# Optimization experiments

Measured on AMD Instinct MI355X. Metric: run time of the kernel, lower is better.

## Reference

```python
import jax, jax.numpy as jnp
import numpy as np

C_IN = 512
C = 64        # per-head dim
N_HEAD = 8
B, S = 2, 2048


def setup_inputs() -> dict:
    key = jax.random.key(0)
    ks = jax.random.split(key, 9)
    scale = 1.0 / np.sqrt(C_IN)
    return {
        "x": jax.random.normal(ks[0], (B, S, C_IN), dtype=jnp.float32),
        "bias": jax.random.normal(ks[1], (B, N_HEAD, S, S), dtype=jnp.float32),
        "Wq": jax.random.normal(ks[2], (N_HEAD * C, C_IN), dtype=jnp.float32) * scale,
        "Wk": jax.random.normal(ks[3], (N_HEAD * C, C_IN), dtype=jnp.float32) * scale,
        "Wv": jax.random.normal(ks[4], (N_HEAD * C, C_IN), dtype=jnp.float32) * scale,
        "Wo": jax.random.normal(ks[5], (C_IN, N_HEAD * C), dtype=jnp.float32) * scale,
        "bo": jax.random.normal(ks[6], (C_IN,), dtype=jnp.float32) * 0.01,
        "Wg": jax.random.normal(ks[7], (N_HEAD * C, C_IN), dtype=jnp.float32) * scale,
        "bg": jax.random.normal(ks[8], (N_HEAD * C,), dtype=jnp.float32) * 0.01,
    }


def reference(x, bias, Wq, Wk, Wv, Wo, bo, Wg, bg):
    # x: [B, S, C_IN]; attn_dim=1 -> q/k/v axis is already at -2 after movedim.
    # Project and split heads: [B, S, H*C] -> [B, H, S, C]
    def split_heads(t):
        Bq, Sq, _ = t.shape
        return t.reshape(Bq, Sq, N_HEAD, C).transpose(0, 2, 1, 3)

    q = split_heads(x @ Wq.T) / jnp.sqrt(jnp.asarray(C, x.dtype))
    k = split_heads(x @ Wk.T)
    v = split_heads(x @ Wv.T)

    a = jnp.einsum("bhqc,bhkc->bhqk", q, k) + bias   # [B, H, S, S]
    a = jax.nn.softmax(a, axis=-1)
    o = jnp.einsum("bhqk,bhkc->bhqc", a, v)          # [B, H, S, C]

    # merge heads back: [B, S, H*C]
    o = o.transpose(0, 2, 1, 3).reshape(x.shape[0], x.shape[1], N_HEAD * C)
    g = jax.nn.sigmoid(x @ Wg.T + bg)
    o = g * o
    return o @ Wo.T + bo                              # [B, S, C_IN]
```

## Files before the change

### kernel.cpp

```cpp
#include <hip/hip_runtime.h>
#include <math.h>

#define BB 2
#define HH 8
#define SS 2048
#define CC 64
#define CIN 512
#define DDIM 512
#define MM (BB*SS)
#define KSPLIT 2
#define KDOM (SS / KSPLIT)
#define NCHUNK (KDOM / 64)

#define SOFTMAX_SHIFT 16.0f

using short8  = __attribute__((ext_vector_type(8))) short;
using float4v = __attribute__((ext_vector_type(4))) float;

__device__ __forceinline__ unsigned short tob(float f) {
    unsigned u = __float_as_uint(f);
    unsigned r = (u + 0x7fffu + ((u >> 16) & 1u)) >> 16;
    return (unsigned short)r;
}
__device__ __forceinline__ float fromb(unsigned short u) {
    return __uint_as_float(((unsigned)u) << 16);
}

__global__ __launch_bounds__(256) void convert_all(
    const float* __restrict__ x,
    const float* __restrict__ wq, const float* __restrict__ wk,
    const float* __restrict__ wv, const float* __restrict__ wg,
    const float* __restrict__ wo,
    unsigned short* __restrict__ xb,
    unsigned short* __restrict__ wqb, unsigned short* __restrict__ wkb,
    unsigned short* __restrict__ wvb, unsigned short* __restrict__ wgb,
    unsigned short* __restrict__ wob)
{
    const int NX4 = MM * CIN / 4;
    int i = blockIdx.x * blockDim.x + threadIdx.x;
    const float* src; unsigned short* dst; float scale = 1.0f; int off;
    if (i < NX4) { src = x; dst = xb; off = i; }
    else {
        int j = i - NX4;
        int seg = j >> 16;
        off = j & 65535;
        if      (seg == 0) { src = wq; dst = wqb; scale = 0.125f; }
        else if (seg == 1) { src = wk; dst = wkb; }
        else if (seg == 2) { src = wv; dst = wvb; }
        else if (seg == 3) { src = wg; dst = wgb; }
        else               { src = wo; dst = wob; }
    }
    float4 v = ((const float4*)src)[off];
    ushort4 o;
    o.x = tob(v.x * scale); o.y = tob(v.y * scale);
    o.z = tob(v.z * scale); o.w = tob(v.w * scale);
    ((ushort4*)dst)[off] = o;
}

__global__ __launch_bounds__(256) void proj_gemm(
    const unsigned short* __restrict__ X,
    const unsigned short* __restrict__ Wq,
    const unsigned short* __restrict__ Wk,
    const unsigned short* __restrict__ Wv,
    const unsigned short* __restrict__ Wg,
    const float* __restrict__ bg,
    unsigned short* __restrict__ Qd,
    unsigned short* __restrict__ Kd,
    unsigned short* __restrict__ Vd,
    unsigned short* __restrict__ Gd)
{
    __shared__ __align__(16) unsigned short At[64][72];
    __shared__ __align__(16) unsigned short Bt[64][72];

    int mode = blockIdx.z;
    const unsigned short* W = (mode == 0) ? Wq : (mode == 1) ? Wk : (mode == 2) ? Wv : Wg;

    int m0 = blockIdx.y * 64;
    int n0 = blockIdx.x * 64;
    int tid = threadIdx.x;
    int w = tid >> 6, lane = tid & 63;
    int quad = lane >> 4, l16 = lane & 15;
    int wm = w & 1, wn = w >> 1;

    float4v acc[2][2];
    for (int a = 0; a < 2; ++a) for (int c = 0; c < 2; ++c) acc[a][c] = (float4v)0.0f;

    for (int kc = 0; kc < CIN; kc += 64) {
        for (int it = 0; it < 2; ++it) {
            int idx = it * 2048 + tid * 8;
            int row = idx >> 6, col = idx & 63;
            *(short8*)&At[row][col] = *(const short8*)&X[(size_t)(m0 + row) * CIN + kc + col];
            *(short8*)&Bt[row][col] = *(const short8*)&W[(size_t)(n0 + row) * CIN + kc + col];
        }
        __syncthreads();
        for (int ks = 0; ks < 2; ++ks) {
            short8 a0 = *(const short8*)&At[wm * 32 + l16][ks * 32 + quad * 8];
            short8 a1 = *(const short8*)&At[wm * 32 + 16 + l16][ks * 32 + quad * 8];
            short8 b0 = *(const short8*)&Bt[wn * 32 + l16][ks * 32 + quad * 8];
            short8 b1 = *(const short8*)&Bt[wn * 32 + 16 + l16][ks * 32 + quad * 8];
            acc[0][0] = __builtin_amdgcn_mfma_f32_16x16x32_bf16(a0, b0, acc[0][0], 0, 0, 0);
            acc[0][1] = __builtin_amdgcn_mfma_f32_16x16x32_bf16(a0, b1, acc[0][1], 0, 0, 0);
            acc[1][0] = __builtin_amdgcn_mfma_f32_16x16x32_bf16(a1, b0, acc[1][0], 0, 0, 0);
            acc[1][1] = __builtin_amdgcn_mfma_f32_16x16x32_bf16(a1, b1, acc[1][1], 0, 0, 0);
        }
        __syncthreads();
    }

    if (mode == 2) {
        for (int a = 0; a < 2; ++a) for (int c = 0; c < 2; ++c)
            for (int r = 0; r < 4; ++r) {
                int ml = wm * 32 + a * 16 + quad * 4 + r;
                int nl = wn * 32 + c * 16 + l16;
                At[nl][ml] = tob(acc[a][c][r]);
            }
        __syncthreads();
        int bi = m0 >> 11, h = n0 >> 6, s0 = m0 & 2047;
        int crow = tid >> 2, seg = tid & 3;
        unsigned short* dp = Vd + (((size_t)(bi * HH + h) * CC) + crow) * SS + s0 + seg * 16;
        *(short8*)dp       = *(const short8*)&At[crow][seg * 16];
        *(short8*)(dp + 8) = *(const short8*)&At[crow][seg * 16 + 8];
        return;
    }

    for (int a = 0; a < 2; ++a) for (int c = 0; c < 2; ++c)
        for (int r = 0; r < 4; ++r) {
            int gm = m0 + wm * 32 + a * 16 + quad * 4 + r;
            int gn = n0 + wn * 32 + c * 16 + l16;
            float v = acc[a][c][r];
            if (mode <= 1) {
                int bi = gm >> 11, s = gm & 2047, h = gn >> 6, cc = gn & 63;
                unsigned short* d = (mode == 0) ? Qd : Kd;
                d[(((size_t)(bi * HH + h) * SS) + s) * CC + cc] = tob(v);
            } else {
                float g = 1.0f / (1.0f + __expf(-(v + bg[gn])));
                Gd[(size_t)gm * DDIM + gn] = tob(g);
            }
        }
}

__global__ __launch_bounds__(256) void attn_kernel(
    const unsigned short* __restrict__ Q,
    const unsigned short* __restrict__ K,
    const unsigned short* __restrict__ V,
    const float* __restrict__ bias,
    float* __restrict__ part,
    float* __restrict__ Ls)
{
    __shared__ __align__(16) unsigned short Kt[64][72];
    __shared__ __align__(16) unsigned short Vt[64][72];
    __shared__ __align__(16) unsigned short Pt[4][16][72];

    int qb = blockIdx.x * 64;
    int bh = blockIdx.y;
    int split = blockIdx.z;
    int ksbase = split * KDOM;
    int b = bh >> 3, h = bh & 7;
    int tid = threadIdx.x;
    int w = tid >> 6, lane = tid & 63;
    int quad = lane >> 4, l16 = lane & 15;

    const unsigned short* Qbh = Q + (size_t)bh * SS * CC;
    const unsigned short* Kbh = K + (size_t)bh * SS * CC + (size_t)ksbase * CC;
    const unsigned short* Vbh = V + (size_t)bh * CC * SS + ksbase;
    const float* biasbh = bias + (size_t)bh * SS * SS + ksbase;

    int qrow = qb + w * 16 + l16;
    short8 aq0 = *(const short8*)&Qbh[(size_t)qrow * CC + quad * 8];
    short8 aq1 = *(const short8*)&Qbh[(size_t)qrow * CC + 32 + quad * 8];

    float lsum[4] = {0.f, 0.f, 0.f, 0.f};
    float4v accO[4];
    for (int jn = 0; jn < 4; ++jn) accO[jn] = (float4v)0.0f;

    int srow0 = (tid * 8) >> 6,        scol0 = (tid * 8) & 63;
    int srow1 = (2048 + tid * 8) >> 6, scol1 = (2048 + tid * 8) & 63;

    const float* brow[4];
    for (int r = 0; r < 4; ++r)
        brow[r] = biasbh + (size_t)(qb + w * 16 + quad * 4 + r) * SS + l16;

    short8 pk0[2], pv0[2], pk1[2], pv1[2];
    float  bb0[4][4], bb1[4][4];
    pk0[0] = *(const short8*)&Kbh[(size_t)srow0 * CC + scol0];
    pk0[1] = *(const short8*)&Kbh[(size_t)srow1 * CC + scol1];
    pv0[0] = *(const short8*)&Vbh[(size_t)srow0 * SS + scol0];
    pv0[1] = *(const short8*)&Vbh[(size_t)srow1 * SS + scol1];
    for (int j = 0; j < 4; ++j)
        for (int r = 0; r < 4; ++r)
            bb0[j][r] = brow[r][j * 16];

#pragma unroll
    for (int c = 0; c < NCHUNK; ++c) {
        int kb  = c * 64;
        int kbn = (c + 1 < NCHUNK ? c + 1 : c) * 64;
        const bool even = (c & 1) == 0;
        short8* pkc = even ? pk0 : pk1;
        short8* pvc = even ? pv0 : pv1;
        short8* pkn = even ? pk1 : pk0;
        short8* pvn = even ? pv1 : pv0;
        float (*bbc)[4] = even ? bb0 : bb1;
        float (*bbn)[4] = even ? bb1 : bb0;

        __syncthreads();
        *(short8*)&Kt[srow0][scol0] = pkc[0];
        *(short8*)&Kt[srow1][scol1] = pkc[1];
        *(short8*)&Vt[srow0][scol0] = pvc[0];
        *(short8*)&Vt[srow1][scol1] = pvc[1];

        pkn[0] = *(const short8*)&Kbh[(size_t)(kbn + srow0) * CC + scol0];
        pkn[1] = *(const short8*)&Kbh[(size_t)(kbn + srow1) * CC + scol1];
        pvn[0] = *(const short8*)&Vbh[(size_t)srow0 * SS + kbn + scol0];
        pvn[1] = *(const short8*)&Vbh[(size_t)srow1 * SS + kbn + scol1];
        for (int j = 0; j < 4; ++j)
            for (int r = 0; r < 4; ++r)
                bbn[j][r] = brow[r][kbn + j * 16];

        __syncthreads();

        float4v sa[4];
        for (int j = 0; j < 4; ++j) sa[j] = (float4v)0.0f;
        for (int j = 0; j < 4; ++j) {
            short8 bk0 = *(const short8*)&Kt[j * 16 + l16][quad * 8];
            short8 bk1 = *(const short8*)&Kt[j * 16 + l16][32 + quad * 8];
            sa[j] = __builtin_amdgcn_mfma_f32_16x16x32_bf16(aq0, bk0, sa[j], 0, 0, 0);
            sa[j] = __builtin_amdgcn_mfma_f32_16x16x32_bf16(aq1, bk1, sa[j], 0, 0, 0);
        }

        for (int j = 0; j < 4; ++j)
            for (int r = 0; r < 4; ++r) {
                float p = __expf(sa[j][r] + bbc[j][r] - SOFTMAX_SHIFT);
                lsum[r] += p;
                Pt[w][quad * 4 + r][j * 16 + l16] = tob(p);
            }

        for (int ks = 0; ks < 2; ++ks) {
            short8 ap = *(const short8*)&Pt[w][l16][ks * 32 + quad * 8];
            for (int jn = 0; jn < 4; ++jn) {
                short8 bv = *(const short8*)&Vt[jn * 16 + l16][ks * 32 + quad * 8];
                accO[jn] = __builtin_amdgcn_mfma_f32_16x16x32_bf16(ap, bv, accO[jn], 0, 0, 0);
            }
        }
    }

    for (int r = 0; r < 4; ++r) {
        float s = lsum[r];
        s += __shfl_xor(s, 1, 64);
        s += __shfl_xor(s, 2, 64);
        s += __shfl_xor(s, 4, 64);
        s += __shfl_xor(s, 8, 64);
        lsum[r] = s;
    }

    int mrow = b * SS + qb + w * 16 + quad * 4;
    float* pOut = part + (size_t)split * MM * DDIM;
    for (int jn = 0; jn < 4; ++jn)
        for (int r = 0; r < 4; ++r)
            pOut[(size_t)(mrow + r) * DDIM + h * 64 + jn * 16 + l16] = accO[jn][r];
    if (l16 == 0)
        for (int r = 0; r < 4; ++r)
            Ls[((size_t)split * MM + mrow + r) * HH + h] = lsum[r];
}

__global__ __launch_bounds__(256) void combine_kernel(
    const float* __restrict__ part,
    const float* __restrict__ Ls,
    const unsigned short* __restrict__ G,
    unsigned short* __restrict__ Og)
{
    int i = blockIdx.x * 256 + threadIdx.x;
    int row = i >> 7;
    int c4  = (i & 127) << 2;
    int h   = c4 >> 6;
    float l = Ls[(size_t)row * HH + h] + Ls[((size_t)MM + row) * HH + h];
    float rl = 1.0f / l;
    const float4* p0 = (const float4*)(part) + ((size_t)row * DDIM + c4) / 4;
    const float4* p1 = (const float4*)(part + (size_t)MM * DDIM) + ((size_t)row * DDIM + c4) / 4;
    float4 a = *p0, bq = *p1;
    ushort4 g = *(const ushort4*)&G[(size_t)row * DDIM + c4];
    ushort4 o;
    o.x = tob((a.x + bq.x) * rl * fromb(g.x));
    o.y = tob((a.y + bq.y) * rl * fromb(g.y));
    o.z = tob((a.z + bq.z) * rl * fromb(g.z));
    o.w = tob((a.w + bq.w) * rl * fromb(g.w));
    *(ushort4*)&Og[(size_t)row * DDIM + c4] = o;
}

__global__ __launch_bounds__(256) void out_gemm(
    const unsigned short* __restrict__ Og,
    const unsigned short* __restrict__ W,
    const float* __restrict__ bo,
    float* __restrict__ out)
{
    __shared__ __align__(16) unsigned short At[64][72];
    __shared__ __align__(16) unsigned short Bt[64][72];

    int m0 = blockIdx.y * 64;
    int n0 = blockIdx.x * 64;
    int tid = threadIdx.x;
    int w = tid >> 6, lane = tid & 63;
    int quad = lane >> 4, l16 = lane & 15;
    int wm = w & 1, wn = w >> 1;

    float4v acc[2][2];
    for (int a = 0; a < 2; ++a) for (int c = 0; c < 2; ++c) acc[a][c] = (float4v)0.0f;

    for (int kc = 0; kc < DDIM; kc += 64) {
        for (int it = 0; it < 2; ++it) {
            int idx = it * 2048 + tid * 8;
            int row = idx >> 6, col = idx & 63;
            *(short8*)&At[row][col] = *(const short8*)&Og[(size_t)(m0 + row) * DDIM + kc + col];
            *(short8*)&Bt[row][col] = *(const short8*)&W[(size_t)(n0 + row) * DDIM + kc + col];
        }
        __syncthreads();
        for (int ks = 0; ks < 2; ++ks) {
            short8 a0 = *(const short8*)&At[wm * 32 + l16][ks * 32 + quad * 8];
            short8 a1 = *(const short8*)&At[wm * 32 + 16 + l16][ks * 32 + quad * 8];
            short8 b0 = *(const short8*)&Bt[wn * 32 + l16][ks * 32 + quad * 8];
            short8 b1 = *(const short8*)&Bt[wn * 32 + 16 + l16][ks * 32 + quad * 8];
            acc[0][0] = __builtin_amdgcn_mfma_f32_16x16x32_bf16(a0, b0, acc[0][0], 0, 0, 0);
            acc[0][1] = __builtin_amdgcn_mfma_f32_16x16x32_bf16(a0, b1, acc[0][1], 0, 0, 0);
            acc[1][0] = __builtin_amdgcn_mfma_f32_16x16x32_bf16(a1, b0, acc[1][0], 0, 0, 0);
            acc[1][1] = __builtin_amdgcn_mfma_f32_16x16x32_bf16(a1, b1, acc[1][1], 0, 0, 0);
        }
        __syncthreads();
    }

    for (int a = 0; a < 2; ++a) for (int c = 0; c < 2; ++c)
        for (int r = 0; r < 4; ++r) {
            int gm = m0 + wm * 32 + a * 16 + quad * 4 + r;
            int gn = n0 + wn * 32 + c * 16 + l16;
            out[(size_t)gm * DDIM + gn] = acc[a][c][r] + bo[gn];
        }
}

extern "C" void kernel_launch(void* const* d_in, const int* in_sizes, int n_in,
                              void* d_out, int out_size, void* d_ws, size_t ws_size,
                              hipStream_t stream)
{
    const float* x    = (const float*)d_in[0];
    const float* bias = (const float*)d_in[1];
    const float* Wq   = (const float*)d_in[2];
    const float* Wk   = (const float*)d_in[3];
    const float* Wv   = (const float*)d_in[4];
    const float* Wo   = (const float*)d_in[5];
    const float* bo   = (const float*)d_in[6];
    const float* Wg   = (const float*)d_in[7];
    const float* bg   = (const float*)d_in[8];
    float* out = (float*)d_out;

    char* ws = (char*)d_ws;
    auto alloc = [&](size_t bytes) { char* p = ws; ws += (bytes + 255) & ~(size_t)255; return p; };
    unsigned short* xb  = (unsigned short*)alloc((size_t)MM * CIN * 2);
    unsigned short* wqb = (unsigned short*)alloc((size_t)DDIM * CIN * 2);
    unsigned short* wkb = (unsigned short*)alloc((size_t)DDIM * CIN * 2);
    unsigned short* wvb = (unsigned short*)alloc((size_t)DDIM * CIN * 2);
    unsigned short* wgb = (unsigned short*)alloc((size_t)DDIM * CIN * 2);
    unsigned short* wob = (unsigned short*)alloc((size_t)DDIM * CIN * 2);
    unsigned short* Qh  = (unsigned short*)alloc((size_t)BB * HH * SS * CC * 2);
    unsigned short* Kh  = (unsigned short*)alloc((size_t)BB * HH * SS * CC * 2);
    unsigned short* Vh  = (unsigned short*)alloc((size_t)BB * HH * SS * CC * 2);
    unsigned short* Gt  = (unsigned short*)alloc((size_t)MM * DDIM * 2);
    unsigned short* Om  = (unsigned short*)alloc((size_t)MM * DDIM * 2);
    float* part = (float*)alloc((size_t)KSPLIT * MM * DDIM * 4);
    float* Lsum = (float*)alloc((size_t)KSPLIT * MM * HH * 4);

    convert_all<<<3328, 256, 0, stream>>>(x, Wq, Wk, Wv, Wg, Wo,
                                          xb, wqb, wkb, wvb, wgb, wob);
    proj_gemm<<<dim3(DDIM / 64, MM / 64, 4), 256, 0, stream>>>(
        xb, wqb, wkb, wvb, wgb, bg, Qh, Kh, Vh, Gt);
    attn_kernel<<<dim3(SS / 64, BB * HH, KSPLIT), 256, 0, stream>>>(
        Qh, Kh, Vh, bias, part, Lsum);
    combine_kernel<<<(MM * DDIM / 4) / 256, 256, 0, stream>>>(part, Lsum, Gt, Om);
    out_gemm<<<dim3(DDIM / 64, MM / 64), 256, 0, stream>>>(Om, wob, bo, out);
}
```

Baseline: 432.4 us.

## Split attention keys four ways, prefetch bias two chunks ahead, use exp2

Raises the key-dimension split from 2 to 4, which doubles the attention grid and raises occupancy. The combine kernel is generalised to sum any number of partials, at the cost of more partial-buffer traffic. The bias is now prefetched two chunks ahead with a triple buffer to hide global-load latency on the dominant bias stream. The softmax switches to hardware exp2: log2e is folded into the Q weight scale and into the bias load with an fma, removing a multiply per element. The extra register buffers may reduce occupancy.

```diff
diff --git a/kernel.cpp b/kernel.cpp
--- a/kernel.cpp
+++ b/kernel.cpp
@@ -8,11 +8,12 @@
 #define CIN 512
 #define DDIM 512
 #define MM (BB*SS)
-#define KSPLIT 2
+#define KSPLIT 4
 #define KDOM (SS / KSPLIT)
 #define NCHUNK (KDOM / 64)
 
-#define SOFTMAX_SHIFT 16.0f
+#define LOG2E 1.4426950408889634f
+#define SHIFT2 (16.0f * LOG2E)
 
 using short8  = __attribute__((ext_vector_type(8))) short;
 using float4v = __attribute__((ext_vector_type(4))) float;
@@ -44,7 +45,7 @@
         int j = i - NX4;
         int seg = j >> 16;
         off = j & 65535;
-        if      (seg == 0) { src = wq; dst = wqb; scale = 0.125f; }
+        if      (seg == 0) { src = wq; dst = wqb; scale = 0.125f * LOG2E; }
         else if (seg == 1) { src = wk; dst = wkb; }
         else if (seg == 2) { src = wv; dst = wvb; }
         else if (seg == 3) { src = wg; dst = wgb; }
@@ -162,7 +163,8 @@
     const unsigned short* Qbh = Q + (size_t)bh * SS * CC;
     const unsigned short* Kbh = K + (size_t)bh * SS * CC + (size_t)ksbase * CC;
     const unsigned short* Vbh = V + (size_t)bh * CC * SS + ksbase;
-    const float* biasbh = bias + (size_t)bh * SS * SS + ksbase;
+    const float* brow0 = bias + (size_t)bh * SS * SS
+                       + (size_t)(qb + w * 16 + quad * 4) * SS + ksbase + l16;
 
     int qrow = qb + w * 16 + l16;
     short8 aq0 = *(const short8*)&Qbh[(size_t)qrow * CC + quad * 8];
@@ -175,50 +177,53 @@
     int srow0 = (tid * 8) >> 6,        scol0 = (tid * 8) & 63;
     int srow1 = (2048 + tid * 8) >> 6, scol1 = (2048 + tid * 8) & 63;
 
-    const float* brow[4];
-    for (int r = 0; r < 4; ++r)
-        brow[r] = biasbh + (size_t)(qb + w * 16 + quad * 4 + r) * SS + l16;
-
-    short8 pk0[2], pv0[2], pk1[2], pv1[2];
-    float  bb0[4][4], bb1[4][4];
-    pk0[0] = *(const short8*)&Kbh[(size_t)srow0 * CC + scol0];
-    pk0[1] = *(const short8*)&Kbh[(size_t)srow1 * CC + scol1];
-    pv0[0] = *(const short8*)&Vbh[(size_t)srow0 * SS + scol0];
-    pv0[1] = *(const short8*)&Vbh[(size_t)srow1 * SS + scol1];
+    short8 pk[2][2], pv[2][2];
+    float  bb[3][4][4];
+    pk[0][0] = *(const short8*)&Kbh[(size_t)srow0 * CC + scol0];
+    pk[0][1] = *(const short8*)&Kbh[(size_t)srow1 * CC + scol1];
+    pv[0][0] = *(const short8*)&Vbh[(size_t)srow0 * SS + scol0];
+    pv[0][1] = *(const short8*)&Vbh[(size_t)srow1 * SS + scol1];
+#pragma unroll
     for (int j = 0; j < 4; ++j)
+#pragma unroll
         for (int r = 0; r < 4; ++r)
-            bb0[j][r] = brow[r][j * 16];
+            bb[0][j][r] = fmaf(brow0[r * SS + j * 16], LOG2E, -SHIFT2);
+#pragma unroll
+    for (int j = 0; j < 4; ++j)
+#pragma unroll
+        for (int r = 0; r < 4; ++r)
+            bb[1][j][r] = fmaf(brow0[r * SS + 64 + j * 16], LOG2E, -SHIFT2);
 
 #pragma unroll
     for (int c = 0; c < NCHUNK; ++c) {
-        int kb  = c * 64;
-        int kbn = (c + 1 < NCHUNK ? c + 1 : c) * 64;
-        const bool even = (c & 1) == 0;
-        short8* pkc = even ? pk0 : pk1;
-        short8* pvc = even ? pv0 : pv1;
-        short8* pkn = even ? pk1 : pk0;
-        short8* pvn = even ? pv1 : pv0;
-        float (*bbc)[4] = even ? bb0 : bb1;
-        float (*bbn)[4] = even ? bb1 : bb0;
-
-        __syncthreads();
-        *(short8*)&Kt[srow0][scol0] = pkc[0];
-        *(short8*)&Kt[srow1][scol1] = pkc[1];
-        *(short8*)&Vt[srow0][scol0] = pvc[0];
-        *(short8*)&Vt[srow1][scol1] = pvc[1];
-
-        pkn[0] = *(const short8*)&Kbh[(size_t)(kbn + srow0) * CC + scol0];
-        pkn[1] = *(const short8*)&Kbh[(size_t)(kbn + srow1) * CC + scol1];
-        pvn[0] = *(const short8*)&Vbh[(size_t)srow0 * SS + kbn + scol0];
-        pvn[1] = *(const short8*)&Vbh[(size_t)srow1 * SS + kbn + scol1];
-        for (int j = 0; j < 4; ++j)
-            for (int r = 0; r < 4; ++r)
-                bbn[j][r] = brow[r][kbn + j * 16];
+        __syncthreads();
+        *(short8*)&Kt[srow0][scol0] = pk[c & 1][0];
+        *(short8*)&Kt[srow1][scol1] = pk[c & 1][1];
+        *(short8*)&Vt[srow0][scol0] = pv[c & 1][0];
+        *(short8*)&Vt[srow1][scol1] = pv[c & 1][1];
+
+        if (c + 1 < NCHUNK) {
+            int kbn = (c + 1) * 64;
+            pk[(c + 1) & 1][0] = *(const short8*)&Kbh[(size_t)(kbn + srow0) * CC + scol0];
+            pk[(c + 1) & 1][1] = *(const short8*)&Kbh[(size_t)(kbn + srow1) * CC + scol1];
+            pv[(c + 1) & 1][0] = *(const short8*)&Vbh[(size_t)srow0 * SS + kbn + scol0];
+            pv[(c + 1) & 1][1] = *(const short8*)&Vbh[(size_t)srow1 * SS + kbn + scol1];
+        }
+        if (c + 2 < NCHUNK) {
+            int kbb = (c + 2) * 64;
+#pragma unroll
+            for (int j = 0; j < 4; ++j)
+#pragma unroll
+                for (int r = 0; r < 4; ++r)
+                    bb[(c + 2) % 3][j][r] = fmaf(brow0[r * SS + kbb + j * 16], LOG2E, -SHIFT2);
+        }
 
         __syncthreads();
 
         float4v sa[4];
+#pragma unroll
         for (int j = 0; j < 4; ++j) sa[j] = (float4v)0.0f;
+#pragma unroll
         for (int j = 0; j < 4; ++j) {
             short8 bk0 = *(const short8*)&Kt[j * 16 + l16][quad * 8];
             short8 bk1 = *(const short8*)&Kt[j * 16 + l16][32 + quad * 8];
@@ -226,15 +231,19 @@
             sa[j] = __builtin_amdgcn_mfma_f32_16x16x32_bf16(aq1, bk1, sa[j], 0, 0, 0);
         }
 
+#pragma unroll
         for (int j = 0; j < 4; ++j)
+#pragma unroll
             for (int r = 0; r < 4; ++r) {
-                float p = __expf(sa[j][r] + bbc[j][r] - SOFTMAX_SHIFT);
+                float p = __builtin_amdgcn_exp2f(sa[j][r] + bb[c % 3][j][r]);
                 lsum[r] += p;
                 Pt[w][quad * 4 + r][j * 16 + l16] = tob(p);
             }
 
+#pragma unroll
         for (int ks = 0; ks < 2; ++ks) {
             short8 ap = *(const short8*)&Pt[w][l16][ks * 32 + quad * 8];
+#pragma unroll
             for (int jn = 0; jn < 4; ++jn) {
                 short8 bv = *(const short8*)&Vt[jn * 16 + l16][ks * 32 + quad * 8];
                 accO[jn] = __builtin_amdgcn_mfma_f32_16x16x32_bf16(ap, bv, accO[jn], 0, 0, 0);
@@ -271,17 +280,23 @@
     int row = i >> 7;
     int c4  = (i & 127) << 2;
     int h   = c4 >> 6;
-    float l = Ls[(size_t)row * HH + h] + Ls[((size_t)MM + row) * HH + h];
+    float l = 0.f;
+#pragma unroll
+    for (int s = 0; s < KSPLIT; ++s)
+        l += Ls[((size_t)s * MM + row) * HH + h];
     float rl = 1.0f / l;
-    const float4* p0 = (const float4*)(part) + ((size_t)row * DDIM + c4) / 4;
-    const float4* p1 = (const float4*)(part + (size_t)MM * DDIM) + ((size_t)row * DDIM + c4) / 4;
-    float4 a = *p0, bq = *p1;
+    float ax = 0.f, ay = 0.f, az = 0.f, aw = 0.f;
+#pragma unroll
+    for (int s = 0; s < KSPLIT; ++s) {
+        float4 t = *(const float4*)(part + (size_t)s * MM * DDIM + (size_t)row * DDIM + c4);
+        ax += t.x; ay += t.y; az += t.z; aw += t.w;
+    }
     ushort4 g = *(const ushort4*)&G[(size_t)row * DDIM + c4];
     ushort4 o;
-    o.x = tob((a.x + bq.x) * rl * fromb(g.x));
-    o.y = tob((a.y + bq.y) * rl * fromb(g.y));
-    o.z = tob((a.z + bq.z) * rl * fromb(g.z));
-    o.w = tob((a.w + bq.w) * rl * fromb(g.w));
+    o.x = tob(ax * rl * fromb(g.x));
+    o.y = tob(ay * rl * fromb(g.y));
+    o.z = tob(az * rl * fromb(g.z));
+    o.w = tob(aw * rl * fromb(g.w));
     *(ushort4*)&Og[(size_t)row * DDIM + c4] = o;
 }
 
```

New measurement: 515.0 us. 1.19x slower.
